# Kernel tuning notes

Measured on AMD Instinct MI355X. Metric: run time of the kernel, lower is better.

## Reference

```python
import jax, jax.numpy as jnp
import numpy as np

N_BINS = 20  # matches ECELoss_DRL(n_bins=20)


def setup_inputs() -> dict:
    key = jax.random.key(0)
    k1, k2 = jax.random.split(key)
    N, C = 1_000_000, 128
    logits = jax.random.normal(k1, (N, C), dtype=jnp.float32)
    softmaxes = jax.nn.softmax(logits, axis=-1)  # valid probabilities in (0,1]
    labels = jax.random.randint(k2, (N,), 0, C, dtype=jnp.int32)
    return {"softmaxes": softmaxes, "labels": labels}


def reference(softmaxes, labels):
    # torch.max(softmaxes, 1) -> (confidences, predictions)
    conf = jnp.max(softmaxes, axis=1)                  # [N]
    pred = jnp.argmax(softmaxes, axis=1)               # [N]
    acc = (pred == labels).astype(jnp.float32)         # [N]
    n = softmaxes.shape[0]

    # Bin b covers (b/n_bins, (b+1)/n_bins] -> single-pass bucketize replacing
    # the 20-iteration python loop of gt/le masks.
    bin_idx = jnp.clip(jnp.ceil(conf * N_BINS).astype(jnp.int32) - 1, 0, N_BINS - 1)

    ones = jnp.ones_like(conf)
    counts = jax.ops.segment_sum(ones, bin_idx, num_segments=N_BINS)    # [20]
    conf_sum = jax.ops.segment_sum(conf, bin_idx, num_segments=N_BINS)  # [20]
    acc_sum = jax.ops.segment_sum(acc, bin_idx, num_segments=N_BINS)    # [20]

    nonempty = counts > 0
    safe = jnp.maximum(counts, 1.0)
    avg_conf = conf_sum / safe
    avg_acc = acc_sum / safe
    prop = counts / n  # prop_in_bin = in_bin.float().mean()

    ece = jnp.sum(jnp.where(nonempty, jnp.abs(avg_conf - avg_acc) * prop, 0.0)).reshape(1)
    ys = jnp.where(nonempty, avg_acc, 0.0)  # per-bin accuracies, 0 for empty bins
    return ece, ys
```

## Files before the change

### kernel.cpp

```cpp
#include <hip/hip_runtime.h>

#define NBINS 20
#define C 128


__global__ __launch_bounds__(256) void ece_pass1(
    const float* __restrict__ sm, const int* __restrict__ labels, int N,
    double* __restrict__ g_csum, unsigned* __restrict__ g_cnt,
    unsigned* __restrict__ g_cor) {
  __shared__ float s_csum[NBINS];
  __shared__ unsigned s_cnt[NBINS];
  __shared__ unsigned s_cor[NBINS];
  const int tid = threadIdx.x;
  if (tid < NBINS) { s_csum[tid] = 0.f; s_cnt[tid] = 0u; s_cor[tid] = 0u; }
  __syncthreads();

  const int lane = tid & 63;
  const int p = lane & 7;
  const int r = lane >> 3;
  const long long gw     = (long long)blockIdx.x * 4 + (tid >> 6);
  const long long stride = (long long)gridDim.x * 4 * 16;

  for (long long base = gw * 16; base < N; base += stride) {
    float4 v[2][4];
#pragma unroll
    for (int g = 0; g < 2; ++g) {
      const long long row = base + g * 8 + r;
      if (row < N) {
        const float4* rp = (const float4*)(sm + row * (long long)C);
#pragma unroll
        for (int k = 0; k < 4; ++k) v[g][k] = rp[p + k * 8];
      } else {
#pragma unroll
        for (int k = 0; k < 4; ++k) v[g][k] = make_float4(-2.f, -2.f, -2.f, -2.f);
      }
    }

#pragma unroll
    for (int g = 0; g < 2; ++g) {
      float bv = -3.f;
      int bi = 0;
#pragma unroll
      for (int k = 0; k < 4; ++k) {
        const float4 q = v[g][k];
        const int b0 = k * 32 + p * 4;
        if (q.x > bv) { bv = q.x; bi = b0; }
        if (q.y > bv) { bv = q.y; bi = b0 + 1; }
        if (q.z > bv) { bv = q.z; bi = b0 + 2; }
        if (q.w > bv) { bv = q.w; bi = b0 + 3; }
      }
#pragma unroll
      for (int off = 1; off <= 4; off <<= 1) {
        const float ov = __shfl_xor(bv, off);
        const int   oi = __shfl_xor(bi, off);
        if (ov > bv || (ov == bv && oi < bi)) { bv = ov; bi = oi; }
      }
      const long long row = base + g * 8 + r;
      if (p == 0 && row < N) {
        int bin = (int)ceilf(bv * 20.0f) - 1;
        bin = min(max(bin, 0), NBINS - 1);
        atomicAdd(&s_csum[bin], bv);
        atomicAdd(&s_cnt[bin], 1u);
        if (bi == labels[row]) atomicAdd(&s_cor[bin], 1u);
      }
    }
  }
  __syncthreads();
  if (tid < NBINS && s_cnt[tid]) {
    atomicAdd(&g_cnt[tid], s_cnt[tid]);
    atomicAdd(&g_cor[tid], s_cor[tid]);
    atomicAdd(&g_csum[tid], (double)s_csum[tid]);
  }
}

__global__ void ece_pass2(const double* __restrict__ g_csum,
                          const unsigned* __restrict__ g_cnt,
                          const unsigned* __restrict__ g_cor,
                          float* __restrict__ out, int N) {
  const int i = threadIdx.x;
  double contrib = 0.0;
  if (i < NBINS) {
    const unsigned c = g_cnt[i];
    const double safe = c ? (double)c : 1.0;
    const double avg_conf = g_csum[i] / safe;
    const double avg_acc  = (double)g_cor[i] / safe;
    out[1 + i] = c ? (float)avg_acc : 0.f;
    if (c) contrib = fabs(avg_conf - avg_acc) * ((double)c / (double)N);
  }
#pragma unroll
  for (int off = 16; off >= 1; off >>= 1) contrib += __shfl_down(contrib, off);
  if (i == 0) out[0] = (float)contrib;
}

extern "C" void kernel_launch(void* const* d_in, const int* in_sizes, int n_in,
                              void* d_out, int out_size, void* d_ws, size_t ws_size,
                              hipStream_t stream) {
  const float* sm     = (const float*)d_in[0];
  const int*   labels = (const int*)d_in[1];
  const int N = in_sizes[1];

  double*   g_csum = (double*)d_ws;
  unsigned* g_cnt  = (unsigned*)((char*)d_ws + NBINS * sizeof(double));
  unsigned* g_cor  = g_cnt + NBINS;

  hipMemsetAsync(d_ws, 0, NBINS * sizeof(double) + 2 * NBINS * sizeof(unsigned),
                 stream);

  ece_pass1<<<2048, 256, 0, stream>>>(sm, labels, N, g_csum, g_cnt, g_cor);
  ece_pass2<<<1, 64, 0, stream>>>(g_csum, g_cnt, g_cor, (float*)d_out, N);
}
```

Measured before the change: 655.7 us.

## Software-pipeline row loads with nontemporal loads and packed shared-memory counters

Restructures the main loop into a double-buffered pipeline: the next 8-row group (including its label) is loaded before the current one is processed, and loads use nontemporal hints. The count and correct-count shared atomics are packed into one 32-bit counter (low and high 16 bits), halving those LDS atomics. Label loads are hoisted into the issue step. The packed counter is only safe while each block handles fewer than 65536 rows per bin. That holds here, at about 500 rows per block.

```diff
diff --git a/kernel.cpp b/kernel.cpp
--- a/kernel.cpp
+++ b/kernel.cpp
@@ -2,6 +2,8 @@
 
 #define NBINS 20
 #define C 128
+
+typedef float vf4 __attribute__((ext_vector_type(4)));
 
 
 __global__ __launch_bounds__(256) void ece_pass1(
@@ -9,67 +11,88 @@
     double* __restrict__ g_csum, unsigned* __restrict__ g_cnt,
     unsigned* __restrict__ g_cor) {
   __shared__ float s_csum[NBINS];
-  __shared__ unsigned s_cnt[NBINS];
-  __shared__ unsigned s_cor[NBINS];
+  __shared__ unsigned s_cc[NBINS];
   const int tid = threadIdx.x;
-  if (tid < NBINS) { s_csum[tid] = 0.f; s_cnt[tid] = 0u; s_cor[tid] = 0u; }
+  if (tid < NBINS) { s_csum[tid] = 0.f; s_cc[tid] = 0u; }
   __syncthreads();
 
   const int lane = tid & 63;
   const int p = lane & 7;
   const int r = lane >> 3;
-  const long long gw     = (long long)blockIdx.x * 4 + (tid >> 6);
-  const long long stride = (long long)gridDim.x * 4 * 16;
 
-  for (long long base = gw * 16; base < N; base += stride) {
-    float4 v[2][4];
+  const long long gw   = (long long)blockIdx.x * 4 + (tid >> 6);
+  const long long hstr = (long long)gridDim.x * 4 * 2;
+  const long long nh   = ((long long)N + 7) >> 3;
+
+  vf4 va[4], vb[4];
+  int la = 0, lb = 0;
+
+  auto issue = [&](long long hh, vf4 (&v)[4], int& lab) {
+    const long long row = hh * 8 + r;
+    if (row < (long long)N) {
+      const vf4* rp = (const vf4*)(sm + row * (long long)C);
 #pragma unroll
-    for (int g = 0; g < 2; ++g) {
-      const long long row = base + g * 8 + r;
-      if (row < N) {
-        const float4* rp = (const float4*)(sm + row * (long long)C);
+      for (int k = 0; k < 4; ++k)
+        v[k] = __builtin_nontemporal_load(rp + p + k * 8);
+      lab = labels[row];
+    } else {
 #pragma unroll
-        for (int k = 0; k < 4; ++k) v[g][k] = rp[p + k * 8];
-      } else {
+      for (int k = 0; k < 4; ++k) v[k] = (vf4){-2.f, -2.f, -2.f, -2.f};
+      lab = -1;
+    }
+  };
+
+  auto process = [&](long long hh, const vf4 (&v)[4], int lab) {
+    float bv = -3.f;
+    int bi = 0;
 #pragma unroll
-        for (int k = 0; k < 4; ++k) v[g][k] = make_float4(-2.f, -2.f, -2.f, -2.f);
-      }
+    for (int k = 0; k < 4; ++k) {
+      const vf4 q = v[k];
+      const int b0 = k * 32 + p * 4;
+      if (q.x > bv) { bv = q.x; bi = b0; }
+      if (q.y > bv) { bv = q.y; bi = b0 + 1; }
+      if (q.z > bv) { bv = q.z; bi = b0 + 2; }
+      if (q.w > bv) { bv = q.w; bi = b0 + 3; }
     }
+#pragma unroll
+    for (int off = 1; off <= 4; off <<= 1) {
+      const float ov = __shfl_xor(bv, off);
+      const int   oi = __shfl_xor(bi, off);
+      if (ov > bv || (ov == bv && oi < bi)) { bv = ov; bi = oi; }
+    }
+    const long long row = hh * 8 + r;
+    if (p == 0 && row < (long long)N) {
+      int bin = (int)ceilf(bv * 20.0f) - 1;
+      bin = min(max(bin, 0), NBINS - 1);
+      atomicAdd(&s_csum[bin], bv);
+      atomicAdd(&s_cc[bin], 1u + ((bi == lab) ? 0x10000u : 0u));
+    }
+  };
 
-#pragma unroll
-    for (int g = 0; g < 2; ++g) {
-      float bv = -3.f;
-      int bi = 0;
-#pragma unroll
-      for (int k = 0; k < 4; ++k) {
-        const float4 q = v[g][k];
-        const int b0 = k * 32 + p * 4;
-        if (q.x > bv) { bv = q.x; bi = b0; }
-        if (q.y > bv) { bv = q.y; bi = b0 + 1; }
-        if (q.z > bv) { bv = q.z; bi = b0 + 2; }
-        if (q.w > bv) { bv = q.w; bi = b0 + 3; }
-      }
-#pragma unroll
-      for (int off = 1; off <= 4; off <<= 1) {
-        const float ov = __shfl_xor(bv, off);
-        const int   oi = __shfl_xor(bi, off);
-        if (ov > bv || (ov == bv && oi < bi)) { bv = ov; bi = oi; }
-      }
-      const long long row = base + g * 8 + r;
-      if (p == 0 && row < N) {
-        int bin = (int)ceilf(bv * 20.0f) - 1;
-        bin = min(max(bin, 0), NBINS - 1);
-        atomicAdd(&s_csum[bin], bv);
-        atomicAdd(&s_cnt[bin], 1u);
-        if (bi == labels[row]) atomicAdd(&s_cor[bin], 1u);
-      }
+  long long h = gw * 2;
+  long long hn = h + 1;
+  issue(h, va, la);
+
+  while (h < nh) {
+    issue(hn, vb, lb);
+    process(h, va, la);
+    h = hn;
+    hn = (h & 1) ? (h + hstr - 1) : (h + 1);
+    if (h >= nh) break;
+    issue(hn, va, la);
+    process(h, vb, lb);
+    h = hn;
+    hn = (h & 1) ? (h + hstr - 1) : (h + 1);
+  }
+
+  __syncthreads();
+  if (tid < NBINS) {
+    const unsigned cc = s_cc[tid];
+    if (cc) {
+      atomicAdd(&g_cnt[tid], cc & 0xFFFFu);
+      atomicAdd(&g_cor[tid], cc >> 16);
+      atomicAdd(&g_csum[tid], (double)s_csum[tid]);
     }
-  }
-  __syncthreads();
-  if (tid < NBINS && s_cnt[tid]) {
-    atomicAdd(&g_cnt[tid], s_cnt[tid]);
-    atomicAdd(&g_cor[tid], s_cor[tid]);
-    atomicAdd(&g_csum[tid], (double)s_csum[tid]);
   }
 }
 
@@ -103,8 +126,9 @@
   unsigned* g_cnt  = (unsigned*)((char*)d_ws + NBINS * sizeof(double));
   unsigned* g_cor  = g_cnt + NBINS;
 
-  hipMemsetAsync(d_ws, 0, NBINS * sizeof(double) + 2 * NBINS * sizeof(unsigned),
-                 stream);
+  (void)hipMemsetAsync(d_ws, 0,
+                       NBINS * sizeof(double) + 2 * NBINS * sizeof(unsigned),
+                       stream);
 
   ece_pass1<<<2048, 256, 0, stream>>>(sm, labels, N, g_csum, g_cnt, g_cor);
   ece_pass2<<<1, 64, 0, stream>>>(g_csum, g_cnt, g_cor, (float*)d_out, N);
```

Result: faster. 626.4 us (-4.5%).
